# Kernel optimization log

Measured on AMD Instinct MI355X. Metric: run time of the kernel, lower is better.

Reference implementation:

```python
import jax, jax.numpy as jnp
import numpy as np

B, S, D = 8, 2048, 1024      # batch, seq (tokens), in/out token dim
E = 2 * D                    # expansion dim (expansion_factor=2)
SDIM = 128                   # attention feature dim s
SQRT_S = float(np.sqrt(SDIM))
EPS_LN = 1e-5                # ScaleNorm eps


def setup_inputs() -> dict:
    key = jax.random.key(0)
    ks = jax.random.split(key, 8)
    return {
        "x": jax.random.normal(ks[0], (B, S, D), jnp.float32),
        "pos_enc": jax.random.normal(ks[1], (S, SDIM), jnp.float32),
        "ln_g": jnp.ones((1,), jnp.float32),                                   # ScaleNorm scalar gain
        "uv_w": jax.random.normal(ks[2], (2 * E + SDIM, D), jnp.float32) / np.sqrt(D),  # fused uv proj (xavier-ish)
        "gamma": jax.random.uniform(ks[3], (2, SDIM), jnp.float32),            # q/k affine scale
        "beta": jax.random.uniform(ks[4], (2, SDIM), jnp.float32),             # q/k affine shift
        "o_w": jax.random.normal(ks[5], (D, E), jnp.float32) / np.sqrt(E),     # output proj
        "res_scale": jnp.ones((D,), jnp.float32),                              # ChannelWiseScale
    }


def reference(x, pos_enc, ln_g, uv_w, gamma, beta, o_w, res_scale):
    # ScaleNorm: x / clamp(||x|| * d^-0.5, eps) * g
    norm = jnp.linalg.norm(x, axis=-1, keepdims=True) * (D ** -0.5)
    xn = x / jnp.maximum(norm, EPS_LN) * ln_g
    # fused uv projection + SiLU
    uv = jax.nn.silu(xn @ uv_w.T)                      # [B,S,2E+s]
    u = uv[..., :E]                                    # gate
    v = uv[..., E:2 * E]                               # values
    base = uv[..., 2 * E:]                             # shared q/k base [B,S,s]
    qk_base = base[..., None, :] * gamma + beta        # [B,S,2,s]
    q = qk_base[..., 0, :] + pos_enc                   # add positional enc [B,S,s]
    k = qk_base[..., 1, :] + pos_enc
    # squared-ReLU attention kernel
    kernel = jnp.square(jax.nn.relu(jnp.einsum('bqs,bks->bqk', q, k) / SQRT_S))
    out = (u * jnp.einsum('bqk,bke->bqe', kernel, v)) @ o_w.T  # [B,S,D]
    # channel-wise scaled residual (in_dims == out_dims -> shortcut)
    return x * res_scale + out
```

## Files before the change

kernel.cpp:

```cpp
#include <hip/hip_runtime.h>
#include <stdint.h>

#define B_   8
#define S_   2048
#define D_   1024
#define E_   2048
#define SD_  128
#define M_   (B_ * S_)
#define NUV  (2 * E_ + SD_)
#define NUV2 4352

typedef __attribute__((ext_vector_type(8))) short short8;
typedef __attribute__((ext_vector_type(4))) float floatx4;

typedef __attribute__((address_space(1))) void as1_void;
typedef __attribute__((address_space(3))) void as3_void;

__device__ __forceinline__ ushort f2bf(float f) {
    uint32_t u = __float_as_uint(f);
    uint32_t r = (u + 0x7fffu + ((u >> 16) & 1u)) >> 16;
    return (ushort)r;
}
__device__ __forceinline__ float bf2f(ushort h) {
    return __uint_as_float(((uint32_t)h) << 16);
}
__device__ __forceinline__ float silu(float z) {
    return z * __builtin_amdgcn_rcpf(1.0f + __expf(-z));
}
__device__ __forceinline__ void gld_lds16(const ushort* g, ushort* l) {
    __builtin_amdgcn_global_load_lds((const as1_void*)g, (as3_void*)l, 16, 0, 0);
}

__device__ __forceinline__ void tile_swizzle4(int& mt, int& nt) {
    const int gx  = gridDim.x;
    const int lin = blockIdx.y * gx + blockIdx.x;
    const int bandSz = gx * 4;
    const int band = lin / bandSz;
    const int rem  = lin - band * bandSz;
    const int full = gx >> 2;
    const int sc   = rem >> 4;
    if (sc < full) {
        const int r2 = rem & 15;
        mt = band * 4 + (r2 & 3);
        nt = sc * 4 + (r2 >> 2);
    } else {
        const int r3 = rem - full * 16;
        mt = band * 4 + (r3 & 3);
        nt = full * 4 + (r3 >> 2);
    }
}

#define STAGE_A(bufn, h, kk) { \
    gld_lds16(gA0 + (size_t)(h) * a128 + (kk), LA##bufn + (h) * 8192 + t * 8); \
    gld_lds16(gA1 + (size_t)(h) * a128 + (kk), LA##bufn + (h) * 8192 + t * 8 + 4096); }
#define STAGE_B(bufn, h, kk) { \
    gld_lds16(gB0 + (size_t)(h) * b128 + (kk), LB##bufn + (h) * 8192 + t * 8); \
    gld_lds16(gB1 + (size_t)(h) * b128 + (kk), LB##bufn + (h) * 8192 + t * 8 + 4096); }

#define PHASE(bufn, mq, nq, STAGES, WAITC) { \
    short8 af_[4][2], bf_[2][2]; \
    { const ushort* pa_ = LA##bufn + (mq) * 8192 + aoff; \
      const ushort* pb_ = LB##bufn + (nq) * 8192 + boff; \
      _Pragma("unroll") \
      for (int mi_ = 0; mi_ < 4; ++mi_) { \
          af_[mi_][0] = *(const short8*)(pa_ + mi_ * 1024 + koff0); \
          af_[mi_][1] = *(const short8*)(pa_ + mi_ * 1024 + koff1); } \
      _Pragma("unroll") \
      for (int ni_ = 0; ni_ < 2; ++ni_) { \
          bf_[ni_][0] = *(const short8*)(pb_ + ni_ * 1024 + koff0); \
          bf_[ni_][1] = *(const short8*)(pb_ + ni_ * 1024 + koff1); } } \
    STAGES \
    __builtin_amdgcn_s_barrier(); \
    asm volatile("s_waitcnt lgkmcnt(0)" ::: "memory"); \
    __builtin_amdgcn_sched_barrier(0); \
    __builtin_amdgcn_s_setprio(1); \
    _Pragma("unroll") \
    for (int mi_ = 0; mi_ < 4; ++mi_) \
        _Pragma("unroll") \
        for (int ni_ = 0; ni_ < 2; ++ni_) { \
            acc[mq][nq][mi_][ni_] = __builtin_amdgcn_mfma_f32_16x16x32_bf16( \
                af_[mi_][0], bf_[ni_][0], acc[mq][nq][mi_][ni_], 0, 0, 0); \
            acc[mq][nq][mi_][ni_] = __builtin_amdgcn_mfma_f32_16x16x32_bf16( \
                af_[mi_][1], bf_[ni_][1], acc[mq][nq][mi_][ni_], 0, 0, 0); } \
    __builtin_amdgcn_s_setprio(0); \
    WAITC \
    __builtin_amdgcn_s_barrier(); }

__device__ __forceinline__ void gemm256(
    const ushort* __restrict__ A, const ushort* __restrict__ B,
    int lda, int ldb, int K, int m0, int n0,
    ushort* lds, floatx4 (&acc)[2][2][4][2])
{
    const int t    = threadIdx.x;
    const int lane = t & 63;
    const int l15  = lane & 15;
    const int quad = lane >> 4;
    const int w    = t >> 6;
    const int wr   = w >> 2;
    const int wc   = w & 3;
    const int key  = l15 & 7;
    const int aoff  = (wr * 64 + l15) * 64;
    const int boff  = (wc * 32 + l15) * 64;
    const int koff0 = (quad ^ key) * 8;
    const int koff1 = ((quad + 4) ^ key) * 8;

    ushort* const LA0 = lds;
    ushort* const LA1 = lds + 16384;
    ushort* const LB0 = lds + 32768;
    ushort* const LB1 = lds + 49152;

    const int r0 = t >> 3;
    const int k0 = ((t & 7) ^ (r0 & 7)) * 8;
    const ushort* gA0 = A + (size_t)(m0 + r0) * lda + k0;
    const ushort* gA1 = gA0 + (size_t)64 * lda;
    const ushort* gB0 = B + (size_t)(n0 + r0) * ldb + k0;
    const ushort* gB1 = gB0 + (size_t)64 * ldb;
    const size_t a128 = (size_t)128 * lda;
    const size_t b128 = (size_t)128 * ldb;

    STAGE_A(0, 0, 0) STAGE_B(0, 0, 0) STAGE_A(0, 1, 0) STAGE_B(0, 1, 0)
    STAGE_A(1, 0, 64) STAGE_B(1, 0, 64)
    asm volatile("s_waitcnt vmcnt(4)" ::: "memory");
    __builtin_amdgcn_s_barrier();

    const int nIter = K >> 7;
    #pragma unroll 1
    for (int i = 0; i < nIter; ++i) {
        const bool lastI = (i == nIter - 1);
        const int kb = i * 128;
        PHASE(0, 0, 0, STAGE_A(1, 1, kb + 64) STAGE_B(1, 1, kb + 64), )
        PHASE(0, 0, 1, , )
        PHASE(0, 1, 0, if (!lastI) { STAGE_A(0, 0, kb + 128) }, )
        PHASE(0, 1, 1, if (!lastI) { STAGE_B(0, 0, kb + 128) },
              if (!lastI) { asm volatile("s_waitcnt vmcnt(4)" ::: "memory"); }
              else        { asm volatile("s_waitcnt vmcnt(0)" ::: "memory"); } )
        PHASE(1, 0, 0, if (!lastI) { STAGE_A(0, 1, kb + 128) STAGE_B(0, 1, kb + 128) }, )
        PHASE(1, 0, 1, , )
        PHASE(1, 1, 0, if (!lastI) { STAGE_A(1, 0, kb + 192) }, )
        PHASE(1, 1, 1, if (!lastI) { STAGE_B(1, 0, kb + 192) },
              if (!lastI) { asm volatile("s_waitcnt vmcnt(4)" ::: "memory"); } )
    }
}

#define ZERO_ACC256 \
    floatx4 acc[2][2][4][2]; \
    _Pragma("unroll") for (int zq_ = 0; zq_ < 2; ++zq_) \
    _Pragma("unroll") for (int zn_ = 0; zn_ < 2; ++zn_) \
    _Pragma("unroll") for (int zm_ = 0; zm_ < 4; ++zm_) \
    _Pragma("unroll") for (int zl_ = 0; zl_ < 2; ++zl_) \
    _Pragma("unroll") for (int zr_ = 0; zr_ < 4; ++zr_) \
        acc[zq_][zn_][zm_][zl_][zr_] = 0.0f;

#define EPI256 \
    const int t = threadIdx.x; \
    const int lane = t & 63, l15 = lane & 15, quad = lane >> 4; \
    const int w = t >> 6, wr = w >> 2, wc = w & 3; \
    (void)t; (void)lane;


__global__ __launch_bounds__(256) void k_cvt(const float* __restrict__ src,
                                             ushort* __restrict__ dst, int n4) {
    int i = blockIdx.x * 256 + threadIdx.x;
    if (i < n4) {
        float4 v = ((const float4*)src)[i];
        ushort4 o;
        o.x = f2bf(v.x); o.y = f2bf(v.y); o.z = f2bf(v.z); o.w = f2bf(v.w);
        ((ushort4*)dst)[i] = o;
    }
}

__global__ __launch_bounds__(256) void k_rmsnorm(const float* __restrict__ x,
                                                 const float* __restrict__ ln_g,
                                                 ushort* __restrict__ xnb) {
    const int m = blockIdx.x;
    const int t = threadIdx.x;
    float4 v = ((const float4*)(x + (size_t)m * D_))[t];
    float ss = v.x * v.x + v.y * v.y + v.z * v.z + v.w * v.w;
    #pragma unroll
    for (int off = 32; off > 0; off >>= 1) ss += __shfl_down(ss, off, 64);
    __shared__ float red[4];
    if ((t & 63) == 0) red[t >> 6] = ss;
    __syncthreads();
    float tot = red[0] + red[1] + red[2] + red[3];
    float rms = sqrtf(tot * (1.0f / (float)D_));
    float scale = ln_g[0] / fmaxf(rms, 1e-5f);
    ushort4 o;
    o.x = f2bf(v.x * scale); o.y = f2bf(v.y * scale);
    o.z = f2bf(v.z * scale); o.w = f2bf(v.w * scale);
    ((ushort4*)(xnb + (size_t)m * D_))[t] = o;
}

__global__ __launch_bounds__(512, 2) void k_gemm1(
    const ushort* __restrict__ xnb, const ushort* __restrict__ uvwb,
    const float* __restrict__ gamma, const float* __restrict__ beta,
    const float* __restrict__ pos,
    ushort* __restrict__ u, ushort* __restrict__ vT,
    ushort* __restrict__ qb, ushort* __restrict__ kb)
{
    __shared__ __align__(16) ushort lds[65536];
    ZERO_ACC256
    int mt, nt;
    tile_swizzle4(mt, nt);
    const int m0 = mt * 256, n0 = nt * 256;
    gemm256(xnb, uvwb, D_, D_, D_, m0, n0, lds, acc);
    EPI256

    if (nt < 8) {
        #pragma unroll
        for (int mq = 0; mq < 2; ++mq)
        #pragma unroll
        for (int nq = 0; nq < 2; ++nq)
        #pragma unroll
        for (int mi = 0; mi < 4; ++mi)
        #pragma unroll
        for (int ni = 0; ni < 2; ++ni) {
            const int col = n0 + nq * 128 + wc * 32 + ni * 16 + l15;
            const int rb  = m0 + mq * 128 + wr * 64 + mi * 16 + quad * 4;
            #pragma unroll
            for (int r = 0; r < 4; ++r)
                u[(size_t)(rb + r) * E_ + col] = f2bf(silu(acc[mq][nq][mi][ni][r]));
        }
    } else if (nt < 16) {
        const int b   = m0 >> 11;
        const int s0q = m0 & (S_ - 1);
        const int ec0 = n0 - E_;
        ushort* vTb = vT + ((size_t)b * E_ + ec0) * S_ + s0q;
        #pragma unroll
        for (int h = 0; h < 2; ++h) {
            __syncthreads();
            #pragma unroll
            for (int mq = 0; mq < 2; ++mq)
            #pragma unroll
            for (int mi = 0; mi < 4; ++mi)
            #pragma unroll
            for (int ni = 0; ni < 2; ++ni) {
                const int e_l = wc * 32 + ni * 16 + l15;
                const int s_l = mq * 128 + wr * 64 + mi * 16 + quad * 4;
                ushort4 pk;
                pk.x = f2bf(silu(acc[mq][h][mi][ni][0]));
                pk.y = f2bf(silu(acc[mq][h][mi][ni][1]));
                pk.z = f2bf(silu(acc[mq][h][mi][ni][2]));
                pk.w = f2bf(silu(acc[mq][h][mi][ni][3]));
                *(ushort4*)&lds[e_l * 264 + s_l] = pk;
            }
            __syncthreads();
            #pragma unroll
            for (int i2 = 0; i2 < 8; ++i2) {
                const int lin = i2 * 512 + t;
                const int e_l = lin >> 5;
                const int sc2 = (lin & 31) * 8;
                *(short8*)(vTb + (size_t)(h * 128 + e_l) * S_ + sc2) =
                    *(const short8*)&lds[e_l * 264 + sc2];
            }
        }
    } else {
        #pragma unroll
        for (int ni = 0; ni < 2; ++ni) {
            const int sd = wc * 32 + ni * 16 + l15;
            const float g0 = gamma[sd], g1 = gamma[SD_ + sd];
            const float be0 = beta[sd], be1 = beta[SD_ + sd];
            #pragma unroll
            for (int mq = 0; mq < 2; ++mq)
            #pragma unroll
            for (int mi = 0; mi < 4; ++mi) {
                const int rb = m0 + mq * 128 + wr * 64 + mi * 16 + quad * 4;
                #pragma unroll
                for (int r = 0; r < 4; ++r) {
                    const int row  = rb + r;
                    const int srow = row & (S_ - 1);
                    const float s = silu(acc[mq][0][mi][ni][r]);
                    const float p = pos[(size_t)srow * SD_ + sd];
                    qb[(size_t)row * SD_ + sd] = f2bf(s * g0 + be0 + p);
                    kb[(size_t)row * SD_ + sd] = f2bf(s * g1 + be1 + p);
                }
            }
        }
    }
}

__global__ __launch_bounds__(512, 2) void k_scores(
    const ushort* __restrict__ qb, const ushort* __restrict__ kb,
    ushort* __restrict__ kern, int b_off)
{
    __shared__ __align__(16) ushort lds[65536];
    ZERO_ACC256
    const int bz = blockIdx.z;
    const int b  = b_off + bz;
    int mt, nt;
    tile_swizzle4(mt, nt);
    const int m0 = mt * 256, n0 = nt * 256;
    gemm256(qb + (size_t)b * S_ * SD_, kb + (size_t)b * S_ * SD_,
            SD_, SD_, SD_, m0, n0, lds, acc);
    EPI256
    ushort* ko = kern + (size_t)bz * S_ * S_;
    const float inv = 0.08838834764831845f;
    #pragma unroll
    for (int mq = 0; mq < 2; ++mq)
    #pragma unroll
    for (int nq = 0; nq < 2; ++nq)
    #pragma unroll
    for (int mi = 0; mi < 4; ++mi)
    #pragma unroll
    for (int ni = 0; ni < 2; ++ni) {
        const int col = n0 + nq * 128 + wc * 32 + ni * 16 + l15;
        const int rb  = m0 + mq * 128 + wr * 64 + mi * 16 + quad * 4;
        #pragma unroll
        for (int r = 0; r < 4; ++r) {
            float s = fmaxf(acc[mq][nq][mi][ni][r] * inv, 0.0f);
            ko[(size_t)(rb + r) * S_ + col] = f2bf(s * s);
        }
    }
}

__global__ __launch_bounds__(512, 2) void k_kv(
    const ushort* __restrict__ kern, const ushort* __restrict__ vT,
    const ushort* __restrict__ u, ushort* __restrict__ kvu, int b_off)
{
    __shared__ __align__(16) ushort lds[65536];
    ZERO_ACC256
    const int bz = blockIdx.z;
    const int b  = b_off + bz;
    int mt, nt;
    tile_swizzle4(mt, nt);
    const int m0 = mt * 256, n0 = nt * 256;
    gemm256(kern + (size_t)bz * S_ * S_, vT + (size_t)b * E_ * S_,
            S_, S_, S_, m0, n0, lds, acc);
    EPI256
    #pragma unroll
    for (int mq = 0; mq < 2; ++mq)
    #pragma unroll
    for (int nq = 0; nq < 2; ++nq)
    #pragma unroll
    for (int mi = 0; mi < 4; ++mi)
    #pragma unroll
    for (int ni = 0; ni < 2; ++ni) {
        const int col = n0 + nq * 128 + wc * 32 + ni * 16 + l15;
        const int rb  = m0 + mq * 128 + wr * 64 + mi * 16 + quad * 4;
        #pragma unroll
        for (int r = 0; r < 4; ++r) {
            const size_t gi = (size_t)(b * S_ + rb + r) * E_ + col;
            float uval = bf2f(u[gi]);
            kvu[gi] = f2bf(uval * acc[mq][nq][mi][ni][r]);
        }
    }
}

__global__ __launch_bounds__(512, 2) void k_out(
    const ushort* __restrict__ kvu, const ushort* __restrict__ owb,
    const float* __restrict__ x, const float* __restrict__ res_scale,
    float* __restrict__ out)
{
    __shared__ __align__(16) ushort lds[65536];
    ZERO_ACC256
    int mt, nt;
    tile_swizzle4(mt, nt);
    const int m0 = mt * 256, n0 = nt * 256;
    gemm256(kvu, owb, E_, E_, E_, m0, n0, lds, acc);
    EPI256
    #pragma unroll
    for (int mq = 0; mq < 2; ++mq)
    #pragma unroll
    for (int nq = 0; nq < 2; ++nq)
    #pragma unroll
    for (int mi = 0; mi < 4; ++mi)
    #pragma unroll
    for (int ni = 0; ni < 2; ++ni) {
        const int col = n0 + nq * 128 + wc * 32 + ni * 16 + l15;
        const float rs = res_scale[col];
        const int rb = m0 + mq * 128 + wr * 64 + mi * 16 + quad * 4;
        #pragma unroll
        for (int r = 0; r < 4; ++r) {
            const size_t gi = (size_t)(rb + r) * D_ + col;
            out[gi] = x[gi] * rs + acc[mq][nq][mi][ni][r];
        }
    }
}

extern "C" void kernel_launch(void* const* d_in, const int* in_sizes, int n_in,
                              void* d_out, int out_size, void* d_ws, size_t ws_size,
                              hipStream_t stream)
{
    const float* x         = (const float*)d_in[0];
    const float* pos       = (const float*)d_in[1];
    const float* ln_g      = (const float*)d_in[2];
    const float* uv_w      = (const float*)d_in[3];
    const float* gamma     = (const float*)d_in[4];
    const float* beta      = (const float*)d_in[5];
    const float* o_w       = (const float*)d_in[6];
    const float* res_scale = (const float*)d_in[7];
    float* out = (float*)d_out;

    char* p = (char*)d_ws;
    ushort* region0 = (ushort*)p; p += (size_t)M_ * D_ * 2;
    ushort* uvwb    = (ushort*)p; p += (size_t)NUV2 * D_ * 2;
    ushort* owb     = (ushort*)p; p += (size_t)D_ * E_ * 2;
    ushort* u       = (ushort*)p; p += (size_t)M_ * E_ * 2;
    ushort* kvu     = (ushort*)p; p += (size_t)M_ * E_ * 2;
    ushort* vT      = (ushort*)p; p += (size_t)M_ * E_ * 2;
    ushort* qb      = (ushort*)p; p += (size_t)M_ * SD_ * 2;
    ushort* kb      = (ushort*)p; p += (size_t)M_ * SD_ * 2;

    ushort* xnb  = region0;
    ushort* kern = region0;

    k_cvt<<<(NUV * D_ / 4 + 255) / 256, 256, 0, stream>>>(uv_w, uvwb, NUV * D_ / 4);
    hipMemsetAsync(uvwb + (size_t)NUV * D_, 0,
                   (size_t)(NUV2 - NUV) * D_ * sizeof(ushort), stream);
    k_cvt<<<(D_ * E_ / 4 + 255) / 256, 256, 0, stream>>>(o_w, owb, D_ * E_ / 4);
    k_rmsnorm<<<M_, 256, 0, stream>>>(x, ln_g, xnb);
    k_gemm1<<<dim3(NUV2 / 256, M_ / 256), 512, 0, stream>>>(
        xnb, uvwb, gamma, beta, pos, u, vT, qb, kb);
    for (int g = 0; g < 2; ++g) {
        k_scores<<<dim3(S_ / 256, S_ / 256, 4), 512, 0, stream>>>(qb, kb, kern, g * 4);
        k_kv<<<dim3(E_ / 256, S_ / 256, 4), 512, 0, stream>>>(kern, vT, u, kvu, g * 4);
    }
    k_out<<<dim3(D_ / 256, M_ / 256), 512, 0, stream>>>(kvu, owb, x, res_scale, out);
}
```

Measured before the change: 595.4 us.

## Restructure GEMM k-loop into two phases per buffer with register-held B fragments

The 256x256 GEMM main loop is reorganised from eight small phases per iteration into four larger ones. Each phase now computes a full 128-row half of the output tile against both N halves. B fragments are loaded into registers once per buffer and reused across the two M halves, which halves the LDS reads of B and the number of barriers. The global-to-LDS staging schedule and vmcnt waits are rearranged to match. The cost is more live registers and larger MFMA bursts between barriers, which gives less room to interleave loads with compute.

```diff
diff --git a/kernel.cpp b/kernel.cpp
--- a/kernel.cpp
+++ b/kernel.cpp
@@ -57,31 +57,60 @@
     gld_lds16(gB0 + (size_t)(h) * b128 + (kk), LB##bufn + (h) * 8192 + t * 8); \
     gld_lds16(gB1 + (size_t)(h) * b128 + (kk), LB##bufn + (h) * 8192 + t * 8 + 4096); }
 
-#define PHASE(bufn, mq, nq, STAGES, WAITC) { \
-    short8 af_[4][2], bf_[2][2]; \
-    { const ushort* pa_ = LA##bufn + (mq) * 8192 + aoff; \
-      const ushort* pb_ = LB##bufn + (nq) * 8192 + boff; \
+#define PHA(bufn, STAGES) { \
+    short8 af_[4][2]; \
+    { const ushort* pa_ = LA##bufn + aoff; \
+      const ushort* pb_ = LB##bufn + boff; \
       _Pragma("unroll") \
       for (int mi_ = 0; mi_ < 4; ++mi_) { \
           af_[mi_][0] = *(const short8*)(pa_ + mi_ * 1024 + koff0); \
           af_[mi_][1] = *(const short8*)(pa_ + mi_ * 1024 + koff1); } \
       _Pragma("unroll") \
+      for (int nq_ = 0; nq_ < 2; ++nq_) \
+      _Pragma("unroll") \
       for (int ni_ = 0; ni_ < 2; ++ni_) { \
-          bf_[ni_][0] = *(const short8*)(pb_ + ni_ * 1024 + koff0); \
-          bf_[ni_][1] = *(const short8*)(pb_ + ni_ * 1024 + koff1); } } \
+          bfv[nq_][ni_][0] = *(const short8*)(pb_ + nq_ * 8192 + ni_ * 1024 + koff0); \
+          bfv[nq_][ni_][1] = *(const short8*)(pb_ + nq_ * 8192 + ni_ * 1024 + koff1); } } \
     STAGES \
     __builtin_amdgcn_s_barrier(); \
     asm volatile("s_waitcnt lgkmcnt(0)" ::: "memory"); \
     __builtin_amdgcn_sched_barrier(0); \
     __builtin_amdgcn_s_setprio(1); \
     _Pragma("unroll") \
+    for (int nq_ = 0; nq_ < 2; ++nq_) \
+    _Pragma("unroll") \
     for (int mi_ = 0; mi_ < 4; ++mi_) \
-        _Pragma("unroll") \
-        for (int ni_ = 0; ni_ < 2; ++ni_) { \
-            acc[mq][nq][mi_][ni_] = __builtin_amdgcn_mfma_f32_16x16x32_bf16( \
-                af_[mi_][0], bf_[ni_][0], acc[mq][nq][mi_][ni_], 0, 0, 0); \
-            acc[mq][nq][mi_][ni_] = __builtin_amdgcn_mfma_f32_16x16x32_bf16( \
-                af_[mi_][1], bf_[ni_][1], acc[mq][nq][mi_][ni_], 0, 0, 0); } \
+    _Pragma("unroll") \
+    for (int ni_ = 0; ni_ < 2; ++ni_) { \
+        acc[0][nq_][mi_][ni_] = __builtin_amdgcn_mfma_f32_16x16x32_bf16( \
+            af_[mi_][0], bfv[nq_][ni_][0], acc[0][nq_][mi_][ni_], 0, 0, 0); \
+        acc[0][nq_][mi_][ni_] = __builtin_amdgcn_mfma_f32_16x16x32_bf16( \
+            af_[mi_][1], bfv[nq_][ni_][1], acc[0][nq_][mi_][ni_], 0, 0, 0); } \
+    __builtin_amdgcn_s_setprio(0); \
+    __builtin_amdgcn_s_barrier(); }
+
+#define PHB(bufn, STAGES, WAITC) { \
+    short8 af_[4][2]; \
+    { const ushort* pa_ = LA##bufn + 8192 + aoff; \
+      _Pragma("unroll") \
+      for (int mi_ = 0; mi_ < 4; ++mi_) { \
+          af_[mi_][0] = *(const short8*)(pa_ + mi_ * 1024 + koff0); \
+          af_[mi_][1] = *(const short8*)(pa_ + mi_ * 1024 + koff1); } } \
+    STAGES \
+    __builtin_amdgcn_s_barrier(); \
+    asm volatile("s_waitcnt lgkmcnt(0)" ::: "memory"); \
+    __builtin_amdgcn_sched_barrier(0); \
+    __builtin_amdgcn_s_setprio(1); \
+    _Pragma("unroll") \
+    for (int nq_ = 0; nq_ < 2; ++nq_) \
+    _Pragma("unroll") \
+    for (int mi_ = 0; mi_ < 4; ++mi_) \
+    _Pragma("unroll") \
+    for (int ni_ = 0; ni_ < 2; ++ni_) { \
+        acc[1][nq_][mi_][ni_] = __builtin_amdgcn_mfma_f32_16x16x32_bf16( \
+            af_[mi_][0], bfv[nq_][ni_][0], acc[1][nq_][mi_][ni_], 0, 0, 0); \
+        acc[1][nq_][mi_][ni_] = __builtin_amdgcn_mfma_f32_16x16x32_bf16( \
+            af_[mi_][1], bfv[nq_][ni_][1], acc[1][nq_][mi_][ni_], 0, 0, 0); } \
     __builtin_amdgcn_s_setprio(0); \
     WAITC \
     __builtin_amdgcn_s_barrier(); }
@@ -118,9 +147,11 @@
     const size_t a128 = (size_t)128 * lda;
     const size_t b128 = (size_t)128 * ldb;
 
-    STAGE_A(0, 0, 0) STAGE_B(0, 0, 0) STAGE_A(0, 1, 0) STAGE_B(0, 1, 0)
-    STAGE_A(1, 0, 64) STAGE_B(1, 0, 64)
-    asm volatile("s_waitcnt vmcnt(4)" ::: "memory");
+    short8 bfv[2][2][2];
+
+    STAGE_A(0, 0, 0) STAGE_A(0, 1, 0) STAGE_B(0, 0, 0) STAGE_B(0, 1, 0)
+    STAGE_A(1, 0, 64) STAGE_B(1, 0, 64) STAGE_B(1, 1, 64)
+    asm volatile("s_waitcnt vmcnt(6)" ::: "memory");
     __builtin_amdgcn_s_barrier();
 
     const int nIter = K >> 7;
@@ -128,17 +159,13 @@
     for (int i = 0; i < nIter; ++i) {
         const bool lastI = (i == nIter - 1);
         const int kb = i * 128;
-        PHASE(0, 0, 0, STAGE_A(1, 1, kb + 64) STAGE_B(1, 1, kb + 64), )
-        PHASE(0, 0, 1, , )
-        PHASE(0, 1, 0, if (!lastI) { STAGE_A(0, 0, kb + 128) }, )
-        PHASE(0, 1, 1, if (!lastI) { STAGE_B(0, 0, kb + 128) },
-              if (!lastI) { asm volatile("s_waitcnt vmcnt(4)" ::: "memory"); }
-              else        { asm volatile("s_waitcnt vmcnt(0)" ::: "memory"); } )
-        PHASE(1, 0, 0, if (!lastI) { STAGE_A(0, 1, kb + 128) STAGE_B(0, 1, kb + 128) }, )
-        PHASE(1, 0, 1, , )
-        PHASE(1, 1, 0, if (!lastI) { STAGE_A(1, 0, kb + 192) }, )
-        PHASE(1, 1, 1, if (!lastI) { STAGE_B(1, 0, kb + 192) },
-              if (!lastI) { asm volatile("s_waitcnt vmcnt(4)" ::: "memory"); } )
+        PHA(0, STAGE_A(1, 1, kb + 64))
+        PHB(0, if (!lastI) { STAGE_A(0, 0, kb + 128) STAGE_B(0, 0, kb + 128) STAGE_B(0, 1, kb + 128) },
+               if (!lastI) { asm volatile("s_waitcnt vmcnt(6)" ::: "memory"); }
+               else        { asm volatile("s_waitcnt vmcnt(0)" ::: "memory"); })
+        PHA(1, if (!lastI) { STAGE_A(0, 1, kb + 128) })
+        PHB(1, if (!lastI) { STAGE_A(1, 0, kb + 192) STAGE_B(1, 0, kb + 192) STAGE_B(1, 1, kb + 192) },
+               if (!lastI) { asm volatile("s_waitcnt vmcnt(6)" ::: "memory"); })
     }
 }
 
```

Result: faster. 560.8 us (-5.8%).
